# Kernel optimization log

Hardware: AMD Instinct MI355X
Metric: run time of the kernel (lower is better)

## Reference

```python
import jax, jax.numpy as jnp
import numpy as np

PI = 3.1415927410125732
N = 4096
L = 1.28e-3          # box side [m]
VEL = 5e-7
RC = 3.15e-6         # Rc = diameter/2
RR = 8e-6
RO = 2.5e-5
RA = np.inf
DT_TRANS = 1.4e-14   # DT (translational diffusion)
DR = 0.0028
GAMMA = 25.0
DT = 0.2             # timestep dt
COLL_ITERS = 30      # fixed cap for collision-resolution do-while (orig caps at 1000)


def setup_inputs() -> dict:
    key = jax.random.key(0)
    ks = jax.random.split(key, 7)
    pos_re = jax.random.uniform(ks[0], (N,), jnp.float32) * L
    pos_im = jax.random.uniform(ks[1], (N,), jnp.float32) * L
    ang = jax.random.uniform(ks[2], (N,), jnp.float32, -PI, PI)
    ori_re = jnp.cos(ang)
    ori_im = jnp.sin(ang)
    deltas = jax.random.uniform(ks[3], (N,), jnp.float32) * 0.5
    rot_noise = jax.random.normal(ks[4], (N,), jnp.float32)
    tn_re = jax.random.normal(ks[5], (N,), jnp.float32)
    tn_im = jax.random.normal(ks[6], (N,), jnp.float32)
    return {"pos_re": pos_re, "pos_im": pos_im, "ori_re": ori_re, "ori_im": ori_im,
            "deltas": deltas, "rot_noise": rot_noise, "tn_re": tn_re, "tn_im": tn_im}


def _wrap(diff):
    # torch get_anglediff wrap: (-2pi,2pi) -> ~(-pi,pi)
    diff = jnp.where(diff <= -PI, jnp.mod(diff, PI), diff)
    return diff - (diff >= PI).astype(diff.dtype) * (2.0 * PI)


def _anglediff(a, b):
    return _wrap(jnp.angle(a) - jnp.angle(b))


def _cossim(a, b):
    # nn.CosineSimilarity(dim=1, eps=1e-14) on view_as_real vectors
    dot = a.real * b.real + a.imag * b.imag
    na = jnp.maximum(jnp.abs(a), 1e-14)
    nb = jnp.maximum(jnp.abs(b), 1e-14)
    return dot / (na * nb)


def _mvc(W, z):
    # real [n,n] mask @ complex [n] vector
    return W @ z.real + 1j * (W @ z.imag)


def _solve_collisions(pos):
    n = pos.shape[0]
    eye_f = jnp.eye(n, dtype=jnp.float32)
    eye_c = eye_f.astype(pos.dtype)

    def step(p):
        diff = p[None, :] - p[:, None] + eye_c  # [i,j] = pos_j - pos_i; diag dummy 1 (nan-safe)
        absd = jnp.abs(diff)
        coll = absd <= (2.0 * RC - eye_f)       # diag threshold negative -> self excluded
        move = jnp.where(coll, diff / jnp.where(coll, absd, 1.0) * ((2.1 * RC - absd) * 0.5), 0.0)
        return p - move.sum(axis=1), coll.sum()

    def body(carry, _):
        p, cont = carry
        p_new, ncoll = step(p)
        p = jnp.where(cont, p_new, p)           # do-while: apply move, then continue if collisions
        return (p, jnp.logical_and(cont, ncoll > 0)), None

    body = jax.checkpoint(body)
    (pos, _), _ = jax.lax.scan(body, (pos, jnp.array(True)), None, length=COLL_ITERS)
    return pos


def _forward(pos_re, pos_im, ori_re, ori_im, deltas, rot_noise, tn_re, tn_im):
    pos = (pos_re + 1j * pos_im).astype(jnp.complex64)
    ori = (ori_re + 1j * ori_im).astype(jnp.complex64)
    n = pos.shape[0]
    eye_b = jnp.eye(n, dtype=bool)

    # pairwise |pos_i - pos_j|; diag made 1 to keep abs() grad-safe (diag is masked out / re-added below)
    dists = jnp.abs(pos[:, None] - pos[None, :] + jnp.eye(n, dtype=pos.dtype))
    mask_rr = (dists <= RR) & ~eye_b              # repulsion zone, self excluded (eye subtracted in orig)
    mask_ro = (dists <= RO + RC) | eye_b          # orientation zone, self included (diag dist 0 in orig)
    mask_ra = (dists <= RA + RC) | eye_b          # Ra = inf -> all ones

    # alpha == 2*pi exactly -> within_view branch skipped (matches original)
    ang = jnp.angle(ori)
    abs_ad = jnp.abs(_wrap(ang[:, None] - ang[None, :]))
    in_front = abs_ad < PI / 2

    Wrr = (mask_rr & in_front).astype(jnp.float32)
    Wro = mask_ro.astype(jnp.float32)
    Wra = mask_ra.astype(jnp.float32)

    n_r = Wrr.sum(axis=1)
    S = _mvc(Wrr, pos) / jnp.maximum(n_r, 1.0) - pos * jnp.sign(n_r)
    d = -S

    n_a = Wra.sum(axis=1)
    cms = _mvc(Wra, pos) / jnp.maximum(n_a, 1.0)
    Ps = cms - pos * jnp.sign(n_a)

    osum = _mvc(Wro, ori)
    left = Ps * jnp.exp(1j * deltas)
    right = Ps * jnp.exp(-1j * deltas)

    # T (=300) >= T_release (=200): choose best turn by cosine similarity
    best = jnp.where(_cossim(left, osum) >= _cossim(right, osum), left, right)

    has_rep = jnp.abs(d) > 0.0
    d_safe = jnp.where(has_rep, d, jnp.ones_like(d))
    att = jnp.where(has_rep, _anglediff(d_safe, ori), _anglediff(best, ori))

    s2dr = np.float32(np.sqrt(2.0 * DR))
    sdt = np.float32(np.sqrt(DT))
    rot = jnp.exp(1j * (DT * GAMMA * DR * jnp.sin(att) + rot_noise * s2dr * sdt))

    # complex standard normal: real/imag each N(0, 1/sqrt(2))
    tnoise = (tn_re + 1j * tn_im) * np.float32(np.sqrt(0.5)) * np.float32(np.sqrt(2.0 * DT_TRANS))
    trans = DT * VEL * ori + tnoise * sdt

    new_pos = _solve_collisions(pos + trans)
    new_ori = ori * rot

    c2r = lambda z: jnp.stack([z.real, z.imag], axis=-1)
    # [5, N, 2]: positions, orientations, orientation_sums, leftturns, rightturns (real views)
    return jnp.stack([c2r(new_pos), c2r(new_ori), c2r(osum), c2r(left), c2r(right)], axis=0)


def reference(pos_re, pos_im, ori_re, ori_im, deltas, rot_noise, tn_re, tn_im):
    return _forward(pos_re, pos_im, ori_re, ori_im, deltas, rot_noise, tn_re, tn_im)
```

## Files before the change

kernel.cpp:

```cpp
#include <hip/hip_runtime.h>

#define NPART 4096
#define PI_F 3.1415927410125732f
#define TWO_PI_F 6.2831854820251465f
#define NBCAP 14336
#define SENT 4096

__device__ __forceinline__ float wrapf(float d) {
    if (d <= -PI_F) {
        d = fmodf(d, PI_F);
        if (d < 0.0f) d += PI_F;
    }
    if (d >= PI_F) d -= TWO_PI_F;
    return d;
}

__global__ __launch_bounds__(512)
void k_interact(const float* __restrict__ pr, const float* __restrict__ pim,
                const float* __restrict__ orr, const float* __restrict__ oim,
                const float* __restrict__ deltas,
                const float* __restrict__ rot_noise,
                const float* __restrict__ tn_re, const float* __restrict__ tn_im,
                float* __restrict__ out,
                float2* __restrict__ recPos, int* __restrict__ recMeta,
                unsigned short* __restrict__ recNbr, int* __restrict__ gcnt) {
    constexpr float RR_F  = 8e-6f;
    constexpr float RR2   = RR_F * RR_F;
    constexpr float ROC_F = (float)(2.5e-5 + 3.15e-6);
    constexpr float ROC2  = ROC_F * ROC_F;
    constexpr float CUT_F = 14.3e-6f;
    constexpr float CUT2  = CUT_F * CUT_F;

    __shared__ float2 lsP[512];
    __shared__ float2 lsO[512];
    __shared__ float rA0[512], rA1[512], rA2[512], rA3[512], rA4[512];
    __shared__ float rB0[512], rB1[512], rB2[512], rB3[512], rB4[512];
    __shared__ float cr_[512], ci_[512];
    __shared__ int ncnt[16];
    __shared__ unsigned short nbrL[16 * 16];

    int tid = threadIdx.x;
    int li = tid & 7, sl = tid >> 3;
    int i0 = blockIdx.x * 16 + li;
    int i1 = i0 + 8;

    if (tid < 16) ncnt[tid] = 0;

    float pxA = pr[i0], pyA = pim[i0], oxA = orr[i0], oyA = oim[i0];
    float pxB = pr[i1], pyB = pim[i1], oxB = orr[i1], oyB = oim[i1];

    float nAr = 0.0f, SAre = 0.0f, SAim = 0.0f, oAre = 0.0f, oAim = 0.0f;
    float nBr = 0.0f, SBre = 0.0f, SBim = 0.0f, oBre = 0.0f, oBim = 0.0f;
    float cs_re = 0.0f, cs_im = 0.0f;

    for (int c = 0; c < 8; ++c) {
        int j0 = c * 512;
        __syncthreads();
        float jr = pr[j0 + tid], ji = pim[j0 + tid];
        lsP[tid] = make_float2(jr, ji);
        lsO[tid] = make_float2(orr[j0 + tid], oim[j0 + tid]);
        cs_re += jr; cs_im += ji;
        __syncthreads();
#pragma unroll
        for (int t = 0; t < 8; ++t) {
            int jj = sl * 8 + ((t + sl) & 7);
            int j = j0 + jj;
            float2 pv = lsP[jj];
            float drA = pxA - pv.x, diA = pyA - pv.y;
            float d2A = drA * drA + diA * diA;
            float drB = pxB - pv.x, diB = pyB - pv.y;
            float d2B = drB * drB + diB * diB;
            if (__any((d2A <= ROC2) | (d2B <= ROC2))) {
                float2 ov = lsO[jj];
                if (d2A <= ROC2) { oAre += ov.x; oAim += ov.y; }
                float dotA = oxA * ov.x + oyA * ov.y;
                if ((d2A <= RR2) & (dotA > 0.0f) & (j != i0)) {
                    nAr += 1.0f; SAre += pv.x; SAim += pv.y;
                }
                if (d2A <= CUT2 && j != i0) {
                    int slot = atomicAdd(&ncnt[li], 1);
                    if (slot < 16) nbrL[li * 16 + slot] = (unsigned short)j;
                }
                if (d2B <= ROC2) { oBre += ov.x; oBim += ov.y; }
                float dotB = oxB * ov.x + oyB * ov.y;
                if ((d2B <= RR2) & (dotB > 0.0f) & (j != i1)) {
                    nBr += 1.0f; SBre += pv.x; SBim += pv.y;
                }
                if (d2B <= CUT2 && j != i1) {
                    int slot = atomicAdd(&ncnt[li + 8], 1);
                    if (slot < 16) nbrL[(li + 8) * 16 + slot] = (unsigned short)j;
                }
            }
        }
    }

    rA0[tid] = nAr; rA1[tid] = SAre; rA2[tid] = SAim; rA3[tid] = oAre; rA4[tid] = oAim;
    rB0[tid] = nBr; rB1[tid] = SBre; rB2[tid] = SBim; rB3[tid] = oBre; rB4[tid] = oBim;
    cr_[tid] = cs_re; ci_[tid] = cs_im;
    __syncthreads();
    for (int s = 256; s >= 8; s >>= 1) {
        if (tid < s) {
            rA0[tid] += rA0[tid + s]; rA1[tid] += rA1[tid + s];
            rA2[tid] += rA2[tid + s]; rA3[tid] += rA3[tid + s];
            rA4[tid] += rA4[tid + s];
            rB0[tid] += rB0[tid + s]; rB1[tid] += rB1[tid + s];
            rB2[tid] += rB2[tid + s]; rB3[tid] += rB3[tid + s];
            rB4[tid] += rB4[tid + s];
            cr_[tid] += cr_[tid + s];  ci_[tid] += ci_[tid + s];
        }
        __syncthreads();
    }
    if (tid < 4) { cr_[tid] += cr_[tid + 4]; ci_[tid] += ci_[tid + 4]; }
    __syncthreads();
    if (tid < 2) { cr_[tid] += cr_[tid + 2]; ci_[tid] += ci_[tid + 2]; }
    __syncthreads();
    if (tid == 0) { cr_[0] += cr_[1]; ci_[0] += ci_[1]; }
    __syncthreads();

    if (tid < 16) {
        int i = blockIdx.x * 16 + tid;
        float n_r, S_re, S_im, o_re, o_im, px, py, ox, oy;
        if (tid < 8) {
            n_r = rA0[tid]; S_re = rA1[tid]; S_im = rA2[tid];
            o_re = rA3[tid]; o_im = rA4[tid];
            px = pxA; py = pyA; ox = oxA; oy = oyA;
        } else {
            int g = tid - 8;
            n_r = rB0[g]; S_re = rB1[g]; S_im = rB2[g];
            o_re = rB3[g]; o_im = rB4[g];
            px = pxB; py = pyB; ox = oxB; oy = oyB;
        }

        float maxnr = fmaxf(n_r, 1.0f);
        float sgn = (n_r > 0.0f) ? 1.0f : 0.0f;
        float Sre = S_re / maxnr - px * sgn;
        float Sim = S_im / maxnr - py * sgn;
        float d_re = -Sre, d_im = -Sim;

        float cmsx = cr_[0] * (1.0f / 4096.0f);
        float cmsy = ci_[0] * (1.0f / 4096.0f);
        float Ps_re = cmsx - px;
        float Ps_im = cmsy - py;

        float dl = deltas[i];
        float cd = cosf(dl), sd = sinf(dl);
        float l_re = Ps_re * cd - Ps_im * sd;
        float l_im = Ps_re * sd + Ps_im * cd;
        float r_re = Ps_re * cd + Ps_im * sd;
        float r_im = Ps_im * cd - Ps_re * sd;

        float nb   = fmaxf(hypotf(o_re, o_im), 1e-14f);
        float na_l = fmaxf(hypotf(l_re, l_im), 1e-14f);
        float na_r = fmaxf(hypotf(r_re, r_im), 1e-14f);
        float csl = (l_re * o_re + l_im * o_im) / (na_l * nb);
        float csr = (r_re * o_re + r_im * o_im) / (na_r * nb);
        float b_re = (csl >= csr) ? l_re : r_re;
        float b_im = (csl >= csr) ? l_im : r_im;

        float ai = atan2f(oy, ox);
        bool has_rep = (d_re != 0.0f) || (d_im != 0.0f);
        float att;
        if (has_rep) att = wrapf(atan2f(d_im, d_re) - ai);
        else         att = wrapf(atan2f(b_im, b_re) - ai);

        constexpr float GDD  = (float)(0.2 * 25.0 * 0.0028);
        constexpr float S2DR = 0.07483314773547883f;
        constexpr float SDT  = 0.44721359549995793f;
        float theta = GDD * sinf(att) + (rot_noise[i] * S2DR) * SDT;
        float rr_ = cosf(theta), ri_ = sinf(theta);

        float no_re = ox * rr_ - oy * ri_;
        float no_im = ox * ri_ + oy * rr_;

        constexpr float DTVEL = (float)(0.2 * 5e-7);
        constexpr float C1 = 0.70710678118654752f;
        constexpr float C2 = 1.6733200530681511e-07f;
        float t_re = DTVEL * ox + ((tn_re[i] * C1) * C2) * SDT;
        float t_im = DTVEL * oy + ((tn_im[i] * C1) * C2) * SDT;
        float p0x = px + t_re, p0y = py + t_im;

        float2* o2 = (float2*)out;
        o2[i]            = make_float2(p0x, p0y);
        o2[1 * 4096 + i] = make_float2(no_re, no_im);
        o2[2 * 4096 + i] = make_float2(o_re, o_im);
        o2[3 * 4096 + i] = make_float2(l_re, l_im);
        o2[4 * 4096 + i] = make_float2(r_re, r_im);

        int c = min(ncnt[tid], 16);
        if (c > 0) {
            int cp = (c + 3) & ~3;
            int slot = atomicAdd(&gcnt[0], 1);
            int eoff = atomicAdd(&gcnt[1], cp);
            if (eoff + cp <= NBCAP) {
                recPos[slot] = make_float2(p0x, p0y);
                recMeta[slot] = i | (c << 12) | (eoff << 17);
                for (int m = 0; m < cp; ++m)
                    recNbr[eoff + m] = (m < c) ? nbrL[tid * 16 + m]
                                               : (unsigned short)SENT;
            } else {
                recPos[slot] = make_float2(p0x, p0y);
                recMeta[slot] = i;
            }
        }
    }
}

__global__ __launch_bounds__(1024)
void k_coll_all(const float2* __restrict__ recPos, const int* __restrict__ recMeta,
                const unsigned short* __restrict__ recNbr,
                const int* __restrict__ gcnt, float* __restrict__ out) {
    constexpr float TWO_RC  = (float)(2.0 * 3.15e-6);
    constexpr float TWO_RC2 = TWO_RC * TWO_RC;
    constexpr float C21RC   = (float)(2.1 * 3.15e-6);

    __shared__ float2 pos[NPART + 2];
    __shared__ __align__(16) unsigned short nbr[NBCAP];
    __shared__ int flg[2];
    __shared__ unsigned bmp[2][132];

    int tid = threadIdx.x;
    int n = gcnt[0];
    int totE = min(gcnt[1], NBCAP);

    int nU4 = (totE + 7) >> 3;
    const uint4* src4 = (const uint4*)recNbr;
    uint4* dst4 = (uint4*)nbr;
    for (int e = tid; e < nU4; e += 1024) dst4[e] = src4[e];

    if (tid < 132) { bmp[0][tid] = 0u; bmp[1][tid] = 0u; }
    if (tid == 0) {
        pos[SENT] = make_float2(1e9f, 1e9f);
        flg[0] = 0; flg[1] = 0;
    }

    float myx[4], myy[4];
    int myi[4], myc[4], myo[4];
#pragma unroll
    for (int s = 0; s < 4; ++s) {
        int slot = s * 1024 + tid;
        myc[s] = 0; myi[s] = SENT; myo[s] = 0;
        if (slot < n) {
            float2 p = recPos[slot];
            int meta = recMeta[slot];
            myx[s] = p.x; myy[s] = p.y;
            myi[s] = meta & 4095;
            myc[s] = (meta >> 12) & 31;
            myo[s] = (unsigned)meta >> 17;
            pos[myi[s]] = p;
        }
    }
    __syncthreads();

    int nq0[4], nq1[4], nq2[4], nq3[4];
    bool pm[4];
#pragma unroll
    for (int s = 0; s < 4; ++s) {
        nq0[s] = SENT; nq1[s] = SENT; nq2[s] = SENT; nq3[s] = SENT;
        pm[s] = true;
        if (myc[s] > 0) {
            uint2 w = *(const uint2*)&nbr[myo[s]];
            nq0[s] = w.x & 0xffff; nq1[s] = w.x >> 16;
            nq2[s] = w.y & 0xffff; nq3[s] = w.y >> 16;
        }
    }

    for (int it = 0; it < 30; ++it) {
        int cur = it & 1, nxt = cur ^ 1;
        if (tid < 132) bmp[nxt][tid] = 0u;

        float nx[4], ny[4];
        int ncs[4];
#pragma unroll
        for (int s = 0; s < 4; ++s) {
            ncs[s] = 0;
            int c = myc[s];
            if (c > 0) {
                bool dirty;
                if (it == 0 || c > 4) {
                    dirty = true;
                } else {
                    unsigned hit = pm[s] ? 1u : 0u;
                    hit |= (bmp[cur][nq0[s] >> 5] >> (nq0[s] & 31)) & 1u;
                    hit |= (bmp[cur][nq1[s] >> 5] >> (nq1[s] & 31)) & 1u;
                    hit |= (bmp[cur][nq2[s] >> 5] >> (nq2[s] & 31)) & 1u;
                    hit |= (bmp[cur][nq3[s] >> 5] >> (nq3[s] & 31)) & 1u;
                    dirty = hit != 0u;
                }
                if (dirty) {
                    float px = myx[s], py = myy[s];
                    float mre = 0.0f, mim = 0.0f;
                    int nc = 0;
                    float2 q0 = pos[nq0[s]], q1 = pos[nq1[s]];
                    float2 q2 = pos[nq2[s]], q3 = pos[nq3[s]];
#define COLL_ONE(q)                                                     \
                    {                                                   \
                        float dr = (q).x - px, di = (q).y - py;         \
                        float d2 = dr * dr + di * di;                   \
                        if (d2 <= TWO_RC2) {                            \
                            float a = sqrtf(d2);                        \
                            float mm = (C21RC - a) * 0.5f / a;          \
                            mre += dr * mm; mim += di * mm; ++nc;       \
                        }                                               \
                    }
                    COLL_ONE(q0) COLL_ONE(q1) COLL_ONE(q2) COLL_ONE(q3)
                    for (int m0 = 4; m0 < c; m0 += 4) {
                        uint2 w = *(const uint2*)&nbr[myo[s] + m0];
                        int j0 = w.x & 0xffff, j1 = w.x >> 16;
                        int j2 = w.y & 0xffff, j3 = w.y >> 16;
                        float2 t0 = pos[j0], t1 = pos[j1], t2 = pos[j2], t3 = pos[j3];
                        COLL_ONE(t0) COLL_ONE(t1) COLL_ONE(t2) COLL_ONE(t3)
                    }
#undef COLL_ONE
                    ncs[s] = nc;
                    nx[s] = px - mre; ny[s] = py - mim;
                }
            }
        }
        __syncthreads();
#pragma unroll
        for (int s = 0; s < 4; ++s) {
            pm[s] = (ncs[s] > 0);
            if (ncs[s] > 0) {
                myx[s] = nx[s]; myy[s] = ny[s];
                pos[myi[s]] = make_float2(nx[s], ny[s]);
                atomicOr(&bmp[nxt][myi[s] >> 5], 1u << (myi[s] & 31));
            }
        }
        int any = ncs[0] | ncs[1] | ncs[2] | ncs[3];
        if (any) flg[it & 1] = 1;
        if (tid == 0) flg[(it + 1) & 1] = 0;
        __syncthreads();
        if (flg[it & 1] == 0) break;
    }

    float2* o2 = (float2*)out;
#pragma unroll
    for (int s = 0; s < 4; ++s)
        if (s * 1024 + tid < n) o2[myi[s]] = make_float2(myx[s], myy[s]);
}

extern "C" void kernel_launch(void* const* d_in, const int* in_sizes, int n_in,
                              void* d_out, int out_size, void* d_ws, size_t ws_size,
                              hipStream_t stream) {
    const float* pos_re = (const float*)d_in[0];
    const float* pos_im = (const float*)d_in[1];
    const float* ori_re = (const float*)d_in[2];
    const float* ori_im = (const float*)d_in[3];
    const float* deltas = (const float*)d_in[4];
    const float* rot_noise = (const float*)d_in[5];
    const float* tn_re = (const float*)d_in[6];
    const float* tn_im = (const float*)d_in[7];
    float* out = (float*)d_out;

    int* gcnt = (int*)d_ws;
    float2* recPos = (float2*)((char*)d_ws + 16);
    int* recMeta   = (int*)(recPos + NPART);
    unsigned short* recNbr = (unsigned short*)(recMeta + NPART);

    hipMemsetAsync(gcnt, 0, 16, stream);
    k_interact<<<256, 512, 0, stream>>>(pos_re, pos_im, ori_re, ori_im,
                                        deltas, rot_noise, tn_re, tn_im,
                                        out, recPos, recMeta, recNbr, gcnt);
    k_coll_all<<<1, 1024, 0, stream>>>(recPos, recMeta, recNbr, gcnt, out);
}
```

Measured before the change: 118.8 us.

## Replace atomic compacted neighbor records with fixed per-particle slots

Drops the global atomic slot/offset allocation and the memset, and writes each particle's first four neighbors to a fixed-index quad array with overflow in a 16-wide per-particle table. The collision kernel reads positions from the output buffer, keeps overflow lists for up to 128 particles in a small shared pool, and falls back to global reads beyond that. It also removes the dirty-bitmap skip, so every particle with neighbors is recomputed each iteration. This trades the atomics, the memset launch and the bitmap bookkeeping for more redundant collision work per iteration and more global/shared loads (all 4096 entries instead of compacted ones).

```diff
diff --git a/kernel.cpp b/kernel.cpp
--- a/kernel.cpp
+++ b/kernel.cpp
@@ -3,7 +3,6 @@
 #define NPART 4096
 #define PI_F 3.1415927410125732f
 #define TWO_PI_F 6.2831854820251465f
-#define NBCAP 14336
 #define SENT 4096
 
 __device__ __forceinline__ float wrapf(float d) {
@@ -22,8 +21,8 @@
                 const float* __restrict__ rot_noise,
                 const float* __restrict__ tn_re, const float* __restrict__ tn_im,
                 float* __restrict__ out,
-                float2* __restrict__ recPos, int* __restrict__ recMeta,
-                unsigned short* __restrict__ recNbr, int* __restrict__ gcnt) {
+                uint2* __restrict__ recQuad, int* __restrict__ recC,
+                unsigned short* __restrict__ recNbr16) {
     constexpr float RR_F  = 8e-6f;
     constexpr float RR2   = RR_F * RR_F;
     constexpr float ROC_F = (float)(2.5e-5 + 3.15e-6);
@@ -187,87 +186,74 @@
         o2[4 * 4096 + i] = make_float2(r_re, r_im);
 
         int c = min(ncnt[tid], 16);
-        if (c > 0) {
+        unsigned q0 = (c > 0) ? nbrL[tid * 16 + 0] : (unsigned)SENT;
+        unsigned q1 = (c > 1) ? nbrL[tid * 16 + 1] : (unsigned)SENT;
+        unsigned q2 = (c > 2) ? nbrL[tid * 16 + 2] : (unsigned)SENT;
+        unsigned q3 = (c > 3) ? nbrL[tid * 16 + 3] : (unsigned)SENT;
+        recQuad[i] = make_uint2(q0 | (q1 << 16), q2 | (q3 << 16));
+        recC[i] = c;
+        if (c > 4) {
             int cp = (c + 3) & ~3;
-            int slot = atomicAdd(&gcnt[0], 1);
-            int eoff = atomicAdd(&gcnt[1], cp);
-            if (eoff + cp <= NBCAP) {
-                recPos[slot] = make_float2(p0x, p0y);
-                recMeta[slot] = i | (c << 12) | (eoff << 17);
-                for (int m = 0; m < cp; ++m)
-                    recNbr[eoff + m] = (m < c) ? nbrL[tid * 16 + m]
+            for (int m = 4; m < cp; ++m)
+                recNbr16[i * 16 + m] = (m < c) ? nbrL[tid * 16 + m]
                                                : (unsigned short)SENT;
-            } else {
-                recPos[slot] = make_float2(p0x, p0y);
-                recMeta[slot] = i;
-            }
         }
     }
 }
 
 __global__ __launch_bounds__(1024)
-void k_coll_all(const float2* __restrict__ recPos, const int* __restrict__ recMeta,
-                const unsigned short* __restrict__ recNbr,
-                const int* __restrict__ gcnt, float* __restrict__ out) {
+void k_coll_all(const uint2* __restrict__ recQuad, const int* __restrict__ recC,
+                const unsigned short* __restrict__ recNbr16,
+                float* __restrict__ out) {
     constexpr float TWO_RC  = (float)(2.0 * 3.15e-6);
     constexpr float TWO_RC2 = TWO_RC * TWO_RC;
     constexpr float C21RC   = (float)(2.1 * 3.15e-6);
 
     __shared__ float2 pos[NPART + 2];
-    __shared__ __align__(16) unsigned short nbr[NBCAP];
+    __shared__ __align__(16) unsigned short pool[128 * 16];
     __shared__ int flg[2];
-    __shared__ unsigned bmp[2][132];
+    __shared__ int poolCnt;
 
     int tid = threadIdx.x;
-    int n = gcnt[0];
-    int totE = min(gcnt[1], NBCAP);
-
-    int nU4 = (totE + 7) >> 3;
-    const uint4* src4 = (const uint4*)recNbr;
-    uint4* dst4 = (uint4*)nbr;
-    for (int e = tid; e < nU4; e += 1024) dst4[e] = src4[e];
-
-    if (tid < 132) { bmp[0][tid] = 0u; bmp[1][tid] = 0u; }
     if (tid == 0) {
         pos[SENT] = make_float2(1e9f, 1e9f);
-        flg[0] = 0; flg[1] = 0;
-    }
-
+        flg[0] = 0; flg[1] = 0; poolCnt = 0;
+    }
+
+    const float2* o2in = (const float2*)out;
     float myx[4], myy[4];
-    int myi[4], myc[4], myo[4];
+    int myc[4], myo[4];
+    int nq0[4], nq1[4], nq2[4], nq3[4];
 #pragma unroll
     for (int s = 0; s < 4; ++s) {
-        int slot = s * 1024 + tid;
-        myc[s] = 0; myi[s] = SENT; myo[s] = 0;
-        if (slot < n) {
-            float2 p = recPos[slot];
-            int meta = recMeta[slot];
-            myx[s] = p.x; myy[s] = p.y;
-            myi[s] = meta & 4095;
-            myc[s] = (meta >> 12) & 31;
-            myo[s] = (unsigned)meta >> 17;
-            pos[myi[s]] = p;
-        }
-    }
-    __syncthreads();
-
-    int nq0[4], nq1[4], nq2[4], nq3[4];
-    bool pm[4];
+        int i = s * 1024 + tid;
+        float2 p = o2in[i];
+        myx[s] = p.x; myy[s] = p.y;
+        pos[i] = p;
+        uint2 q = recQuad[i];
+        nq0[s] = q.x & 0xffff; nq1[s] = q.x >> 16;
+        nq2[s] = q.y & 0xffff; nq3[s] = q.y >> 16;
+        myc[s] = recC[i];
+        myo[s] = -1;
+    }
+    __syncthreads();
+
 #pragma unroll
     for (int s = 0; s < 4; ++s) {
-        nq0[s] = SENT; nq1[s] = SENT; nq2[s] = SENT; nq3[s] = SENT;
-        pm[s] = true;
-        if (myc[s] > 0) {
-            uint2 w = *(const uint2*)&nbr[myo[s]];
-            nq0[s] = w.x & 0xffff; nq1[s] = w.x >> 16;
-            nq2[s] = w.y & 0xffff; nq3[s] = w.y >> 16;
-        }
-    }
+        if (myc[s] > 4) {
+            int r = atomicAdd(&poolCnt, 1);
+            if (r < 128) {
+                int i = s * 1024 + tid;
+                const uint4* src = (const uint4*)&recNbr16[i * 16];
+                uint4* dst = (uint4*)&pool[r * 16];
+                dst[0] = src[0]; dst[1] = src[1];
+                myo[s] = r;
+            }
+        }
+    }
+    __syncthreads();
 
     for (int it = 0; it < 30; ++it) {
-        int cur = it & 1, nxt = cur ^ 1;
-        if (tid < 132) bmp[nxt][tid] = 0u;
-
         float nx[4], ny[4];
         int ncs[4];
 #pragma unroll
@@ -275,55 +261,44 @@
             ncs[s] = 0;
             int c = myc[s];
             if (c > 0) {
-                bool dirty;
-                if (it == 0 || c > 4) {
-                    dirty = true;
-                } else {
-                    unsigned hit = pm[s] ? 1u : 0u;
-                    hit |= (bmp[cur][nq0[s] >> 5] >> (nq0[s] & 31)) & 1u;
-                    hit |= (bmp[cur][nq1[s] >> 5] >> (nq1[s] & 31)) & 1u;
-                    hit |= (bmp[cur][nq2[s] >> 5] >> (nq2[s] & 31)) & 1u;
-                    hit |= (bmp[cur][nq3[s] >> 5] >> (nq3[s] & 31)) & 1u;
-                    dirty = hit != 0u;
-                }
-                if (dirty) {
-                    float px = myx[s], py = myy[s];
-                    float mre = 0.0f, mim = 0.0f;
-                    int nc = 0;
-                    float2 q0 = pos[nq0[s]], q1 = pos[nq1[s]];
-                    float2 q2 = pos[nq2[s]], q3 = pos[nq3[s]];
+                float px = myx[s], py = myy[s];
+                float mre = 0.0f, mim = 0.0f;
+                int nc = 0;
+                float2 q0 = pos[nq0[s]], q1 = pos[nq1[s]];
+                float2 q2 = pos[nq2[s]], q3 = pos[nq3[s]];
 #define COLL_ONE(q)                                                     \
-                    {                                                   \
-                        float dr = (q).x - px, di = (q).y - py;         \
-                        float d2 = dr * dr + di * di;                   \
-                        if (d2 <= TWO_RC2) {                            \
-                            float a = sqrtf(d2);                        \
-                            float mm = (C21RC - a) * 0.5f / a;          \
-                            mre += dr * mm; mim += di * mm; ++nc;       \
-                        }                                               \
-                    }
-                    COLL_ONE(q0) COLL_ONE(q1) COLL_ONE(q2) COLL_ONE(q3)
-                    for (int m0 = 4; m0 < c; m0 += 4) {
-                        uint2 w = *(const uint2*)&nbr[myo[s] + m0];
-                        int j0 = w.x & 0xffff, j1 = w.x >> 16;
-                        int j2 = w.y & 0xffff, j3 = w.y >> 16;
-                        float2 t0 = pos[j0], t1 = pos[j1], t2 = pos[j2], t3 = pos[j3];
-                        COLL_ONE(t0) COLL_ONE(t1) COLL_ONE(t2) COLL_ONE(t3)
-                    }
+                {                                                       \
+                    float dr = (q).x - px, di = (q).y - py;             \
+                    float d2 = dr * dr + di * di;                       \
+                    if (d2 <= TWO_RC2) {                                \
+                        float a = sqrtf(d2);                            \
+                        float mm = (C21RC - a) * 0.5f / a;              \
+                        mre += dr * mm; mim += di * mm; ++nc;           \
+                    }                                                   \
+                }
+                COLL_ONE(q0) COLL_ONE(q1) COLL_ONE(q2) COLL_ONE(q3)
+                for (int m0 = 4; m0 < c; m0 += 4) {
+                    uint2 w;
+                    if (myo[s] >= 0)
+                        w = *(const uint2*)&pool[myo[s] * 16 + m0];
+                    else
+                        w = *(const uint2*)&recNbr16[(s * 1024 + tid) * 16 + m0];
+                    int j0 = w.x & 0xffff, j1 = w.x >> 16;
+                    int j2 = w.y & 0xffff, j3 = w.y >> 16;
+                    float2 t0 = pos[j0], t1 = pos[j1], t2 = pos[j2], t3 = pos[j3];
+                    COLL_ONE(t0) COLL_ONE(t1) COLL_ONE(t2) COLL_ONE(t3)
+                }
 #undef COLL_ONE
-                    ncs[s] = nc;
-                    nx[s] = px - mre; ny[s] = py - mim;
-                }
+                ncs[s] = nc;
+                nx[s] = px - mre; ny[s] = py - mim;
             }
         }
         __syncthreads();
 #pragma unroll
         for (int s = 0; s < 4; ++s) {
-            pm[s] = (ncs[s] > 0);
             if (ncs[s] > 0) {
                 myx[s] = nx[s]; myy[s] = ny[s];
-                pos[myi[s]] = make_float2(nx[s], ny[s]);
-                atomicOr(&bmp[nxt][myi[s] >> 5], 1u << (myi[s] & 31));
+                pos[s * 1024 + tid] = make_float2(nx[s], ny[s]);
             }
         }
         int any = ncs[0] | ncs[1] | ncs[2] | ncs[3];
@@ -336,7 +311,7 @@
     float2* o2 = (float2*)out;
 #pragma unroll
     for (int s = 0; s < 4; ++s)
-        if (s * 1024 + tid < n) o2[myi[s]] = make_float2(myx[s], myy[s]);
+        o2[s * 1024 + tid] = make_float2(myx[s], myy[s]);
 }
 
 extern "C" void kernel_launch(void* const* d_in, const int* in_sizes, int n_in,
@@ -352,14 +327,12 @@
     const float* tn_im = (const float*)d_in[7];
     float* out = (float*)d_out;
 
-    int* gcnt = (int*)d_ws;
-    float2* recPos = (float2*)((char*)d_ws + 16);
-    int* recMeta   = (int*)(recPos + NPART);
-    unsigned short* recNbr = (unsigned short*)(recMeta + NPART);
-
-    hipMemsetAsync(gcnt, 0, 16, stream);
+    uint2* recQuad = (uint2*)d_ws;
+    int* recC = (int*)(recQuad + NPART);
+    unsigned short* recNbr16 = (unsigned short*)(recC + NPART);
+
     k_interact<<<256, 512, 0, stream>>>(pos_re, pos_im, ori_re, ori_im,
                                         deltas, rot_noise, tn_re, tn_im,
-                                        out, recPos, recMeta, recNbr, gcnt);
-    k_coll_all<<<1, 1024, 0, stream>>>(recPos, recMeta, recNbr, gcnt, out);
+                                        out, recQuad, recC, recNbr16);
+    k_coll_all<<<1, 1024, 0, stream>>>(recQuad, recC, recNbr16, out);
 }
```

After: 115.1 us. -3.2%, faster.
